# Kernel optimization log

Measured on AMD Instinct MI355X. Metric: run time of the kernel, lower is better.

## Reference

```python
import jax, jax.numpy as jnp
import numpy as np

H = 128          # image height (raster_settings.image_size)
W = 128          # image width
K = 8            # points per pixel kept in the z-buffer
CHUNK = 256      # point chunk size for streaming top-k merge
RADIUS = 0.02    # NDC splat radius
BIG = 1e10       # sentinel depth for empty / out-of-radius
EPS = 1e-6       # homogeneous-divide eps (transform_points eps)


def setup_inputs() -> dict:
    key = jax.random.key(0)
    kxy, kz = jax.random.split(key)
    B, N = 4, 8192
    # points inside a simple view frustum: z in [1,3], xy within +-0.5*z
    z = jax.random.uniform(kz, (B, N, 1), dtype=jnp.float32, minval=1.0, maxval=3.0)
    xy = jax.random.uniform(kxy, (B, N, 2), dtype=jnp.float32, minval=-1.0, maxval=1.0) * z * 0.5
    points = jnp.concatenate([xy, z], axis=-1)
    # world-to-view: identity (points already generated in view space)
    world_to_view = jnp.eye(4, dtype=jnp.float32)
    # simple perspective projection composed with ndc transform (row-vector convention):
    # q = [f*x, f*y, z, z]; after divide -> (f*x/z, f*y/z, 1); z later replaced by view z
    f = 2.0
    proj_to_ndc = jnp.array([[f, 0., 0., 0.],
                             [0., f, 0., 0.],
                             [0., 0., 1., 1.],
                             [0., 0., 0., 0.]], dtype=jnp.float32)
    return {"points": points, "world_to_view": world_to_view, "proj_to_ndc": proj_to_ndc}


def _transform(points, world_to_view, proj_to_ndc):
    # pytorch3d row-vector homogeneous transform_points with eps-safe divide
    ph = jnp.concatenate([points, jnp.ones_like(points[..., :1])], axis=-1)  # (B,N,4)
    pv = ph @ world_to_view
    view_z = pv[..., 2]
    q = pv @ proj_to_ndc
    w = q[..., 3:4]
    sgn = jnp.where(w >= 0, 1.0, -1.0)
    ndc = q[..., :3] / (sgn * jnp.maximum(jnp.abs(w), EPS))
    # pts_ndc[..., 2] = pts_view[..., 2]
    return ndc.at[..., 2].set(view_z)


def _rasterize(pts_ndc):
    # per-pixel z-buffer of the K nearest (smallest view-z) points whose NDC
    # xy distance^2 to the pixel center is <= radius^2, streamed over point chunks
    B, N, _ = pts_ndc.shape
    px = 1.0 - (2.0 * jnp.arange(W, dtype=jnp.float32) + 1.0) / W  # NDC x of pixel centers
    py = 1.0 - (2.0 * jnp.arange(H, dtype=jnp.float32) + 1.0) / H  # NDC y of pixel centers
    r2 = RADIUS * RADIUS
    n_chunks = N // CHUNK
    pts_c = pts_ndc.reshape(B, n_chunks, CHUNK, 3).transpose(1, 0, 2, 3)  # (S,B,C,3)
    base = (jnp.arange(n_chunks) * CHUNK).astype(jnp.int32)
    z0 = jnp.full((B, H, W, K), BIG, dtype=jnp.float32)
    i0 = jnp.full((B, H, W, K), -1, dtype=jnp.int32)
    d0 = jnp.zeros((B, H, W, K), dtype=jnp.float32)

    def body(carry, inp):
        zb, ib, db = carry
        pc, b0 = inp
        x, y, z = pc[..., 0], pc[..., 1], pc[..., 2]                 # (B,C)
        dx = x[:, None, None, :] - px[None, None, :, None]           # (B,1,W,C)
        dy = y[:, None, None, :] - py[None, :, None, None]           # (B,H,1,C)
        d2 = dx * dx + dy * dy                                        # (B,H,W,C)
        inside = (d2 <= r2) & (z[:, None, None, :] > 0)
        zc = jnp.where(inside, z[:, None, None, :], BIG)
        z_all = jnp.concatenate([zb, zc], axis=-1)                    # (B,H,W,K+C)
        d_all = jnp.concatenate([db, d2], axis=-1)
        neg_z, sel = jax.lax.top_k(-z_all, K)                         # K smallest z
        z_new = -neg_z
        d_new = jnp.take_along_axis(d_all, sel, axis=-1)
        i_old = jnp.take_along_axis(ib, jnp.minimum(sel, K - 1), axis=-1)
        i_new = jnp.where(sel < K, i_old, b0 + sel - K)               # global point ids
        return (z_new, i_new, d_new), None

    (zb, ib, db), _ = jax.lax.scan(body, (z0, i0, d0), (pts_c, base))
    valid = zb < BIG * 0.5
    zbuf = jnp.where(valid, zb, -1.0)
    idx = jnp.where(valid, ib, -1)
    dists2 = jnp.where(valid, db, -1.0)
    return idx, zbuf, dists2


def reference(points, world_to_view, proj_to_ndc):
    pts_ndc = _transform(points, world_to_view, proj_to_ndc)
    idx, zbuf, dists2 = _rasterize(pts_ndc)
    # PointFragments(idx, zbuf, zbuf_idx, dists)
    return idx, zbuf, idx, dists2
```

## Files before the change

### kernel.cpp

```cpp
#include <hip/hip_runtime.h>
#include <cstdint>

#define HD __device__ __forceinline__

constexpr int B = 4, N = 8192, H = 128, W = 128, K = 8;
constexpr float BIGF = 1e10f;
constexpr int TOTPIX = B * H * W;
constexpr int CAPP = 32;

HD bool keyless(float z1, int i1, float z2, int i2) {
    return (z1 < z2) || ((z1 == z2) && (i1 < i2));
}

HD void insert_topk(float nz, int ni, float nd,
                    float (&zk)[K], int (&ik)[K], float (&dk)[K]) {
    bool lt[K];
#pragma unroll
    for (int j = 0; j < K; ++j) lt[j] = keyless(nz, ni, zk[j], ik[j]);
#pragma unroll
    for (int j = K - 1; j >= 1; --j) {
        if (lt[j]) {
            if (lt[j - 1]) { zk[j] = zk[j - 1]; ik[j] = ik[j - 1]; dk[j] = dk[j - 1]; }
            else           { zk[j] = nz;        ik[j] = ni;        dk[j] = nd; }
        }
    }
    if (lt[0]) { zk[0] = nz; ik[0] = ni; dk[0] = nd; }
}

HD void write_out(float* __restrict__ out, int pix,
                  const float (&zk)[K], const int (&ik)[K], const float (&dk)[K]) {
    const size_t S = (size_t)TOTPIX * K;
    size_t off = (size_t)pix * K;
    float fi[K], fz[K], fd[K];
#pragma unroll
    for (int j = 0; j < K; ++j) {
        bool valid = zk[j] < 0.5f * BIGF;
        fi[j] = valid ? (float)ik[j] : -1.0f;
        fz[j] = valid ? zk[j] : -1.0f;
        fd[j] = valid ? dk[j] : -1.0f;
    }
    float4* o0 = reinterpret_cast<float4*>(out + off);
    float4* o1 = reinterpret_cast<float4*>(out + S + off);
    float4* o2 = reinterpret_cast<float4*>(out + 2 * S + off);
    float4* o3 = reinterpret_cast<float4*>(out + 3 * S + off);
    o0[0] = make_float4(fi[0], fi[1], fi[2], fi[3]);
    o0[1] = make_float4(fi[4], fi[5], fi[6], fi[7]);
    o1[0] = make_float4(fz[0], fz[1], fz[2], fz[3]);
    o1[1] = make_float4(fz[4], fz[5], fz[6], fz[7]);
    o2[0] = make_float4(fi[0], fi[1], fi[2], fi[3]);
    o2[1] = make_float4(fi[4], fi[5], fi[6], fi[7]);
    o3[0] = make_float4(fd[0], fd[1], fd[2], fd[3]);
    o3[1] = make_float4(fd[4], fd[5], fd[6], fd[7]);
}

__global__ __launch_bounds__(256) void stage_zero_kernel(
    const float* __restrict__ points, const float* __restrict__ w2v,
    const float* __restrict__ p2n, float4* __restrict__ staged,
    int4* __restrict__ cnt4) {
    __shared__ float lc[16];
    int tid = threadIdx.x;
    if (tid < 16) {
        int r = tid & 3, sel = tid >> 2;
        float v;
        if (sel < 3) {
            int j = (sel == 0) ? 0 : (sel == 1) ? 1 : 3;
            v = w2v[r * 4 + 0] * p2n[0 * 4 + j] + w2v[r * 4 + 1] * p2n[1 * 4 + j] +
                w2v[r * 4 + 2] * p2n[2 * 4 + j] + w2v[r * 4 + 3] * p2n[3 * 4 + j];
        } else {
            v = w2v[r * 4 + 2];
        }
        lc[tid] = v;
    }
    __syncthreads();

    int gid = blockIdx.x * 256 + tid;
    if (gid < TOTPIX / 4) cnt4[gid] = make_int4(0, 0, 0, 0);

    float x = points[(size_t)gid * 3 + 0];
    float y = points[(size_t)gid * 3 + 1];
    float z = points[(size_t)gid * 3 + 2];
    float q0 = x * lc[0]  + y * lc[1]  + z * lc[2]  + lc[3];
    float q1 = x * lc[4]  + y * lc[5]  + z * lc[6]  + lc[7];
    float q3 = x * lc[8]  + y * lc[9]  + z * lc[10] + lc[11];
    float zn = x * lc[12] + y * lc[13] + z * lc[14] + lc[15];
    float sgn = (q3 >= 0.0f) ? 1.0f : -1.0f;
    float den = sgn * fmaxf(fabsf(q3), 1e-6f);
    float xn = q0 / den, yn = q1 / den;
    if (!(zn > 0.0f)) xn = 1e30f;
    staged[gid] = make_float4(xn, yn, zn, __int_as_float(gid & (N - 1)));
}

__global__ __launch_bounds__(256) void bin_kernel(
    const float4* __restrict__ staged, int* __restrict__ cnt,
    float4* __restrict__ entries) {
    int gid = blockIdx.x * 256 + threadIdx.x;
    float4 e = staged[gid];
    if (fabsf(e.x) > 1.013f || fabsf(e.y) > 1.013f) return;
    int b = gid >> 13;

    const float rb = 0.0201f;
    const float r2 = (float)(0.02 * 0.02);
    int wmin = (int)ceilf(((1.0f - e.x) - rb) * 64.0f - 0.5f);
    int wmax = (int)floorf(((1.0f - e.x) + rb) * 64.0f - 0.5f);
    int hmin = (int)ceilf(((1.0f - e.y) - rb) * 64.0f - 0.5f);
    int hmax = (int)floorf(((1.0f - e.y) + rb) * 64.0f - 0.5f);
    wmin = max(wmin, 0); wmax = min(wmax, W - 1);
    hmin = max(hmin, 0); hmax = min(hmax, H - 1);

    for (int h = hmin; h <= hmax; ++h) {
        float py = 1.0f - (2.0f * (float)h + 1.0f) / 128.0f;
        float dy = e.y - py;
        float dy2 = __fmul_rn(dy, dy);
        for (int w = wmin; w <= wmax; ++w) {
            float px = 1.0f - (2.0f * (float)w + 1.0f) / 128.0f;
            float dx = e.x - px;
            float d2 = __fadd_rn(__fmul_rn(dx, dx), dy2);
            if (d2 <= r2) {
                int pix = (b << 14) + (h << 7) + w;
                int pos = atomicAdd(&cnt[pix], 1);
                if (pos < CAPP)
                    entries[(size_t)pos * TOTPIX + pix] =
                        make_float4(e.z, d2, e.w, 0.0f);
            }
        }
    }
}

__global__ __launch_bounds__(256) void select_kernel(
    const int* __restrict__ cnt, const float4* __restrict__ entries,
    float* __restrict__ out) {
    int pix = blockIdx.x * 256 + threadIdx.x;
    int c = cnt[pix];
    if (c > CAPP) c = CAPP;

    float zk[K]; int ik[K]; float dk[K];
#pragma unroll
    for (int j = 0; j < K; ++j) { zk[j] = BIGF; ik[j] = 0x7fffffff; dk[j] = 0.0f; }

    for (int j = 0; j < c; ++j) {
        float4 e = entries[(size_t)j * TOTPIX + pix];
        int pi = __float_as_int(e.z);
        if (keyless(e.x, pi, zk[K - 1], ik[K - 1]))
            insert_topk(e.x, pi, e.y, zk, ik, dk);
    }
    write_out(out, pix, zk, ik, dk);
}

HD void transform_point_full(const float* __restrict__ w2v, const float* __restrict__ p2n,
                             float x, float y, float z,
                             float& xn, float& yn, float& zn) {
    float pv[4];
#pragma unroll
    for (int j = 0; j < 4; ++j)
        pv[j] = x * w2v[0 * 4 + j] + y * w2v[1 * 4 + j] +
                z * w2v[2 * 4 + j] + 1.0f * w2v[3 * 4 + j];
    float viewz = pv[2];
    float q0 = pv[0] * p2n[0] + pv[1] * p2n[4] + pv[2] * p2n[8]  + pv[3] * p2n[12];
    float q1 = pv[0] * p2n[1] + pv[1] * p2n[5] + pv[2] * p2n[9]  + pv[3] * p2n[13];
    float q3 = pv[0] * p2n[3] + pv[1] * p2n[7] + pv[2] * p2n[11] + pv[3] * p2n[15];
    float sgn = (q3 >= 0.0f) ? 1.0f : -1.0f;
    float den = sgn * fmaxf(fabsf(q3), 1e-6f);
    xn = q0 / den; yn = q1 / den; zn = viewz;
}

__global__ __launch_bounds__(256) void brute_kernel(
    const float* __restrict__ points, const float* __restrict__ w2v,
    const float* __restrict__ p2n, float* __restrict__ out) {
    int gid = blockIdx.x * 256 + threadIdx.x;
    int b = gid >> 14;
    float px = 1.0f - (2.0f * (float)(gid & 127) + 1.0f) / 128.0f;
    float py = 1.0f - (2.0f * (float)((gid >> 7) & 127) + 1.0f) / 128.0f;
    const float r2 = (float)(0.02 * 0.02);

    __shared__ float4 sh[256];

    float zk[K]; int ik[K]; float dk[K];
#pragma unroll
    for (int j = 0; j < K; ++j) { zk[j] = BIGF; ik[j] = 0x7fffffff; dk[j] = 0.0f; }

    for (int c = 0; c < N; c += 256) {
        __syncthreads();
        int n = c + threadIdx.x;
        float x = points[((size_t)b * N + n) * 3 + 0];
        float y = points[((size_t)b * N + n) * 3 + 1];
        float z = points[((size_t)b * N + n) * 3 + 2];
        float xn, yn, zn;
        transform_point_full(w2v, p2n, x, y, z, xn, yn, zn);
        sh[threadIdx.x] = make_float4(xn, yn, zn, __int_as_float(n));
        __syncthreads();
        for (int e = 0; e < 256; ++e) {
            float4 pe = sh[e];
            float dx = pe.x - px, dy = pe.y - py;
            float d2 = __fadd_rn(__fmul_rn(dx, dx), __fmul_rn(dy, dy));
            int pi = __float_as_int(pe.w);
            if ((d2 <= r2) && (pe.z > 0.0f) && keyless(pe.z, pi, zk[K - 1], ik[K - 1]))
                insert_topk(pe.z, pi, d2, zk, ik, dk);
        }
    }
    write_out(out, gid, zk, ik, dk);
}

extern "C" void kernel_launch(void* const* d_in, const int* in_sizes, int n_in,
                              void* d_out, int out_size, void* d_ws, size_t ws_size,
                              hipStream_t stream) {
    const float* points = (const float*)d_in[0];
    const float* w2v    = (const float*)d_in[1];
    const float* p2n    = (const float*)d_in[2];
    float* out = (float*)d_out;

    const size_t staged_off = 256 << 10;
    const size_t ent_off    = 1 << 20;
    const size_t need = ent_off + (size_t)CAPP * TOTPIX * sizeof(float4);

    if (ws_size >= need) {
        int* cnt        = (int*)d_ws;
        float4* staged  = (float4*)((char*)d_ws + staged_off);
        float4* entries = (float4*)((char*)d_ws + ent_off);
        stage_zero_kernel<<<(B * N) / 256, 256, 0, stream>>>(points, w2v, p2n,
                                                             staged, (int4*)cnt);
        bin_kernel<<<(B * N) / 256, 256, 0, stream>>>(staged, cnt, entries);
        select_kernel<<<TOTPIX / 256, 256, 0, stream>>>(cnt, entries, out);
    } else {
        brute_kernel<<<(B * H * W) / 256, 256, 0, stream>>>(points, w2v, p2n, out);
    }
}
```

Baseline: 29.09 us.

## Fuse bin and select kernels using a global atomic completion flag

```diff
diff --git a/kernel.cpp b/kernel.cpp
--- a/kernel.cpp
+++ b/kernel.cpp
@@ -7,6 +7,8 @@
 constexpr float BIGF = 1e10f;
 constexpr int TOTPIX = B * H * W;
 constexpr int CAPP = 32;
+constexpr int BIN_BLOCKS = (B * N) / 256;
+constexpr int SEL_BLOCKS = TOTPIX / 256;
 
 HD bool keyless(float z1, int i1, float z2, int i2) {
     return (z1 < z2) || ((z1 == z2) && (i1 < i2));
@@ -56,7 +58,7 @@
 __global__ __launch_bounds__(256) void stage_zero_kernel(
     const float* __restrict__ points, const float* __restrict__ w2v,
     const float* __restrict__ p2n, float4* __restrict__ staged,
-    int4* __restrict__ cnt4) {
+    int4* __restrict__ cnt4, int* __restrict__ flag) {
     __shared__ float lc[16];
     int tid = threadIdx.x;
     if (tid < 16) {
@@ -75,6 +77,7 @@
 
     int gid = blockIdx.x * 256 + tid;
     if (gid < TOTPIX / 4) cnt4[gid] = make_int4(0, 0, 0, 0);
+    if (gid == 0) *flag = 0;
 
     float x = points[(size_t)gid * 3 + 0];
     float y = points[(size_t)gid * 3 + 1];
@@ -90,60 +93,77 @@
     staged[gid] = make_float4(xn, yn, zn, __int_as_float(gid & (N - 1)));
 }
 
-__global__ __launch_bounds__(256) void bin_kernel(
+__global__ __launch_bounds__(256) void bin_select_kernel(
     const float4* __restrict__ staged, int* __restrict__ cnt,
-    float4* __restrict__ entries) {
-    int gid = blockIdx.x * 256 + threadIdx.x;
-    float4 e = staged[gid];
-    if (fabsf(e.x) > 1.013f || fabsf(e.y) > 1.013f) return;
-    int b = gid >> 13;
-
-    const float rb = 0.0201f;
-    const float r2 = (float)(0.02 * 0.02);
-    int wmin = (int)ceilf(((1.0f - e.x) - rb) * 64.0f - 0.5f);
-    int wmax = (int)floorf(((1.0f - e.x) + rb) * 64.0f - 0.5f);
-    int hmin = (int)ceilf(((1.0f - e.y) - rb) * 64.0f - 0.5f);
-    int hmax = (int)floorf(((1.0f - e.y) + rb) * 64.0f - 0.5f);
-    wmin = max(wmin, 0); wmax = min(wmax, W - 1);
-    hmin = max(hmin, 0); hmax = min(hmax, H - 1);
-
-    for (int h = hmin; h <= hmax; ++h) {
-        float py = 1.0f - (2.0f * (float)h + 1.0f) / 128.0f;
-        float dy = e.y - py;
-        float dy2 = __fmul_rn(dy, dy);
-        for (int w = wmin; w <= wmax; ++w) {
-            float px = 1.0f - (2.0f * (float)w + 1.0f) / 128.0f;
-            float dx = e.x - px;
-            float d2 = __fadd_rn(__fmul_rn(dx, dx), dy2);
-            if (d2 <= r2) {
-                int pix = (b << 14) + (h << 7) + w;
-                int pos = atomicAdd(&cnt[pix], 1);
-                if (pos < CAPP)
-                    entries[(size_t)pos * TOTPIX + pix] =
-                        make_float4(e.z, d2, e.w, 0.0f);
+    float4* __restrict__ entries, int* __restrict__ flag,
+    float* __restrict__ out) {
+    int blk = blockIdx.x;
+    int tid = threadIdx.x;
+
+    if (blk < BIN_BLOCKS) {
+        int gid = blk * 256 + tid;
+        float4 e = staged[gid];
+        if (!(fabsf(e.x) > 1.013f || fabsf(e.y) > 1.013f)) {
+            int b = gid >> 13;
+            const float rb = 0.0201f;
+            const float r2 = (float)(0.02 * 0.02);
+            int wmin = (int)ceilf(((1.0f - e.x) - rb) * 64.0f - 0.5f);
+            int wmax = (int)floorf(((1.0f - e.x) + rb) * 64.0f - 0.5f);
+            int hmin = (int)ceilf(((1.0f - e.y) - rb) * 64.0f - 0.5f);
+            int hmax = (int)floorf(((1.0f - e.y) + rb) * 64.0f - 0.5f);
+            wmin = max(wmin, 0); wmax = min(wmax, W - 1);
+            hmin = max(hmin, 0); hmax = min(hmax, H - 1);
+            for (int h = hmin; h <= hmax; ++h) {
+                float py = 1.0f - (2.0f * (float)h + 1.0f) / 128.0f;
+                float dy = e.y - py;
+                float dy2 = __fmul_rn(dy, dy);
+                for (int w = wmin; w <= wmax; ++w) {
+                    float px = 1.0f - (2.0f * (float)w + 1.0f) / 128.0f;
+                    float dx = e.x - px;
+                    float d2 = __fadd_rn(__fmul_rn(dx, dx), dy2);
+                    if (d2 <= r2) {
+                        int pix = (b << 14) + (h << 7) + w;
+                        int pos = atomicAdd(&cnt[pix], 1);
+                        if (pos < CAPP)
+                            entries[(size_t)pos * TOTPIX + pix] =
+                                make_float4(e.z, d2, e.w, 0.0f);
+                    }
+                }
             }
         }
-    }
-}
-
-__global__ __launch_bounds__(256) void select_kernel(
-    const int* __restrict__ cnt, const float4* __restrict__ entries,
-    float* __restrict__ out) {
-    int pix = blockIdx.x * 256 + threadIdx.x;
-    int c = cnt[pix];
-    if (c > CAPP) c = CAPP;
-
-    float zk[K]; int ik[K]; float dk[K];
-#pragma unroll
-    for (int j = 0; j < K; ++j) { zk[j] = BIGF; ik[j] = 0x7fffffff; dk[j] = 0.0f; }
-
-    for (int j = 0; j < c; ++j) {
-        float4 e = entries[(size_t)j * TOTPIX + pix];
-        int pi = __float_as_int(e.z);
-        if (keyless(e.x, pi, zk[K - 1], ik[K - 1]))
-            insert_topk(e.x, pi, e.y, zk, ik, dk);
-    }
-    write_out(out, pix, zk, ik, dk);
+        __threadfence();
+        __syncthreads();
+        if (tid == 0)
+            __hip_atomic_fetch_add(flag, 1, __ATOMIC_RELEASE,
+                                   __HIP_MEMORY_SCOPE_AGENT);
+    } else {
+        if (tid == 0) {
+            long long guard = 0;
+            while (__hip_atomic_load(flag, __ATOMIC_ACQUIRE,
+                                     __HIP_MEMORY_SCOPE_AGENT) < BIN_BLOCKS) {
+                __builtin_amdgcn_s_sleep(2);
+                if (++guard > (1ll << 24)) break;
+            }
+        }
+        __syncthreads();
+        __threadfence();
+
+        int pix = (blk - BIN_BLOCKS) * 256 + tid;
+        int c = cnt[pix];
+        if (c > CAPP) c = CAPP;
+
+        float zk[K]; int ik[K]; float dk[K];
+#pragma unroll
+        for (int j = 0; j < K; ++j) { zk[j] = BIGF; ik[j] = 0x7fffffff; dk[j] = 0.0f; }
+
+        for (int j = 0; j < c; ++j) {
+            float4 e = entries[(size_t)j * TOTPIX + pix];
+            int pi = __float_as_int(e.z);
+            if (keyless(e.x, pi, zk[K - 1], ik[K - 1]))
+                insert_topk(e.x, pi, e.y, zk, ik, dk);
+        }
+        write_out(out, pix, zk, ik, dk);
+    }
 }
 
 HD void transform_point_full(const float* __restrict__ w2v, const float* __restrict__ p2n,
@@ -208,18 +228,20 @@
     const float* p2n    = (const float*)d_in[2];
     float* out = (float*)d_out;
 
-    const size_t staged_off = 256 << 10;
+    const size_t flag_off   = 256 << 10;
+    const size_t staged_off = 512 << 10;
     const size_t ent_off    = 1 << 20;
     const size_t need = ent_off + (size_t)CAPP * TOTPIX * sizeof(float4);
 
     if (ws_size >= need) {
         int* cnt        = (int*)d_ws;
+        int* flag       = (int*)((char*)d_ws + flag_off);
         float4* staged  = (float4*)((char*)d_ws + staged_off);
         float4* entries = (float4*)((char*)d_ws + ent_off);
         stage_zero_kernel<<<(B * N) / 256, 256, 0, stream>>>(points, w2v, p2n,
-                                                             staged, (int4*)cnt);
-        bin_kernel<<<(B * N) / 256, 256, 0, stream>>>(staged, cnt, entries);
-        select_kernel<<<TOTPIX / 256, 256, 0, stream>>>(cnt, entries, out);
+                                                             staged, (int4*)cnt, flag);
+        bin_select_kernel<<<BIN_BLOCKS + SEL_BLOCKS, 256, 0, stream>>>(
+            staged, cnt, entries, flag, out);
     } else {
         brute_kernel<<<(B * H * W) / 256, 256, 0, stream>>>(points, w2v, p2n, out);
     }
```

After: 111.1 us. 3.82x slower.
